# Optimization experiments

Hardware: AMD Instinct MI355X
Metric: run time of the kernel (lower is better)

Reference implementation:

```python
import jax, jax.numpy as jnp
import numpy as np

MARGIN = 0.2
SIMILARITY_WEIGHT = 1.0
PD_EPS = 1e-6   # F.pairwise_distance eps (added to the difference)
COS_EPS = 1e-8  # F.cosine_similarity eps (norm clamp)

B, D = 8192, 256


def setup_inputs() -> dict:
    key = jax.random.key(0)
    k1, k2, k3, k4 = jax.random.split(key, 4)
    anchor = jax.random.normal(k1, (B, D), dtype=jnp.float32)
    positive = jax.random.normal(k2, (B, D), dtype=jnp.float32)
    negative = jax.random.normal(k3, (B, D), dtype=jnp.float32)
    similarity_matrix = jax.random.uniform(k4, (B, B), dtype=jnp.float32)
    return {"anchor": anchor, "positive": positive, "negative": negative,
            "similarity_matrix": similarity_matrix}


def reference(anchor, positive, negative, similarity_matrix):
    # Triplet term: F.pairwise_distance(x1, x2, p=2, eps=1e-6) = ||x1 - x2 + eps||_2
    d_pos = jnp.linalg.norm(anchor - positive + PD_EPS, axis=1)  # [B]
    d_neg = jnp.linalg.norm(anchor - negative + PD_EPS, axis=1)  # [B]
    triplet = jnp.mean(jax.nn.relu(d_pos - d_neg + MARGIN))

    # Pairwise cosine similarity of anchor rows (vectorized matmul form).
    norms = jnp.linalg.norm(anchor, axis=1, keepdims=True)       # [B,1]
    a_hat = anchor / jnp.maximum(norms, COS_EPS)                 # [B,D]
    cos = a_hat @ a_hat.T                                        # [B,B]

    # sum_{i,j} mse(cos_ij, S_ij) / B^2 == mean((cos - S)^2)
    sim_loss = jnp.mean((cos - similarity_matrix) ** 2)

    return triplet + SIMILARITY_WEIGHT * sim_loss
```

## Files before the change

kernel.cpp:

```cpp
#include <hip/hip_runtime.h>
#include <hip/hip_bf16.h>

#define BDIM 8192
#define DDIM 256

typedef __attribute__((ext_vector_type(8))) short  s16x8;
typedef __attribute__((ext_vector_type(4))) float  f32x4;

#define GLOBAL_AS __attribute__((address_space(1)))
#define LDS_AS    __attribute__((address_space(3)))

__device__ __forceinline__ void stage16(const float* g, float* l) {
    __builtin_amdgcn_global_load_lds((const GLOBAL_AS unsigned int*)g,
                                     (LDS_AS unsigned int*)l, 16, 0, 0);
}

__device__ inline ushort f2bf(float x) {
    __hip_bfloat16 h = __float2bfloat16(x);
    ushort u;
    __builtin_memcpy(&u, &h, 2);
    return u;
}

__global__ __launch_bounds__(256) void row_stats(
    const float* __restrict__ A, const float* __restrict__ P,
    const float* __restrict__ N, ushort* __restrict__ Asw,
    float* __restrict__ partial_trip)
{
    __shared__ float tsh[4];
    const int wave = threadIdx.x >> 6;
    const int lane = threadIdx.x & 63;
    const int row  = blockIdx.x * 4 + wave;

    const float4 a = *(reinterpret_cast<const float4*>(A + (size_t)row * DDIM) + lane);
    const float4 p = *(reinterpret_cast<const float4*>(P + (size_t)row * DDIM) + lane);
    const float4 n = *(reinterpret_cast<const float4*>(N + (size_t)row * DDIM) + lane);

    float sa = a.x*a.x + a.y*a.y + a.z*a.z + a.w*a.w;

    float d0 = a.x - p.x + 1e-6f, d1 = a.y - p.y + 1e-6f;
    float d2 = a.z - p.z + 1e-6f, d3 = a.w - p.w + 1e-6f;
    float sp = d0*d0 + d1*d1 + d2*d2 + d3*d3;

    d0 = a.x - n.x + 1e-6f; d1 = a.y - n.y + 1e-6f;
    d2 = a.z - n.z + 1e-6f; d3 = a.w - n.w + 1e-6f;
    float sn = d0*d0 + d1*d1 + d2*d2 + d3*d3;

    #pragma unroll
    for (int off = 32; off > 0; off >>= 1) {
        sa += __shfl_xor(sa, off);
        sp += __shfl_xor(sp, off);
        sn += __shfl_xor(sn, off);
    }

    const float inv = 1.0f / fmaxf(sqrtf(sa), 1e-8f);

    ushort4 hv;
    hv.x = f2bf(a.x * inv);
    hv.y = f2bf(a.y * inv);
    hv.z = f2bf(a.z * inv);
    hv.w = f2bf(a.w * inv);
    const size_t chunk = ((size_t)(row >> 4) * 8 + (lane >> 3)) * 64
                       + (size_t)(((lane >> 1) & 3) * 16 + (row & 15));
    *reinterpret_cast<ushort4*>(Asw + chunk * 8 + (lane & 1) * 4) = hv;

    if (lane == 0)
        tsh[wave] = fmaxf(sqrtf(sp) - sqrtf(sn) + 0.2f, 0.0f);
    __syncthreads();
    if (threadIdx.x == 0)
        partial_trip[blockIdx.x] = tsh[0] + tsh[1] + tsh[2] + tsh[3];
}

__global__ __launch_bounds__(256) void cos_mse(
    const ushort* __restrict__ Asw,
    const float* __restrict__ S, float* __restrict__ partial_sim)
{
    __shared__ float s_tile[128 * 128];
    __shared__ float wsum[4];

    const int tid  = threadIdx.x;
    const int w    = tid >> 6;
    const int lane = tid & 63;

    const int bid = blockIdx.x;
    const int swz = (bid & 7) * 512 + (bid >> 3);
    const int ti  = (swz >> 6) * 128;
    const int tj  = (swz & 63) * 128;

    {
        const int rhalf = lane >> 5;
        const int col16 = lane & 31;
        const float* gsrc = S + (size_t)(ti + w * 2 + rhalf) * BDIM + tj + col16 * 4;
        #pragma unroll
        for (int it = 0; it < 16; ++it)
            stage16(gsrc + (size_t)it * 8 * BDIM, &s_tile[(it * 8 + w * 2) * 128]);
    }

    const int wr = (w >> 1) * 64;
    const int wc = (w & 1) * 64;
    const int fr = lane & 15;
    const int kg = lane >> 4;

    const ushort* ab = Asw + (size_t)((ti + wr) >> 4) * 4096 + (size_t)lane * 8;
    const ushort* bb = Asw + (size_t)((tj + wc) >> 4) * 4096 + (size_t)lane * 8;

    f32x4 acc[4][4] = {};

    #pragma unroll 2
    for (int k32 = 0; k32 < 8; ++k32) {
        s16x8 af[4], bf4[4];
        #pragma unroll
        for (int m = 0; m < 4; ++m)
            af[m] = *reinterpret_cast<const s16x8*>(ab + m * 4096 + k32 * 512);
        #pragma unroll
        for (int n = 0; n < 4; ++n)
            bf4[n] = *reinterpret_cast<const s16x8*>(bb + n * 4096 + k32 * 512);
        #pragma unroll
        for (int m = 0; m < 4; ++m)
            #pragma unroll
            for (int n = 0; n < 4; ++n)
                acc[m][n] = __builtin_amdgcn_mfma_f32_16x16x32_bf16(
                    af[m], bf4[n], acc[m][n], 0, 0, 0);
    }

    __syncthreads();

    float local = 0.0f;
    #pragma unroll
    for (int m = 0; m < 4; ++m) {
        #pragma unroll
        for (int reg = 0; reg < 4; ++reg) {
            const int lr = wr + m * 16 + kg * 4 + reg;
            #pragma unroll
            for (int n = 0; n < 4; ++n) {
                const float d = acc[m][n][reg] - s_tile[lr * 128 + wc + n * 16 + fr];
                local += d * d;
            }
        }
    }

    #pragma unroll
    for (int off = 32; off > 0; off >>= 1)
        local += __shfl_down(local, off);
    if (lane == 0) wsum[w] = local;
    __syncthreads();
    if (tid == 0)
        partial_sim[bid] = wsum[0] + wsum[1] + wsum[2] + wsum[3];
}

__global__ __launch_bounds__(256) void finalize(
    const float* __restrict__ pt, const float* __restrict__ ps,
    float* __restrict__ out)
{
    __shared__ float sh[4];
    float v = 0.0f;
    for (int i = threadIdx.x; i < 2048; i += 256) v += pt[i] * (1.0f / (float)BDIM);
    for (int i = threadIdx.x; i < 4096; i += 256)
        v += ps[i] * (1.0f / ((float)BDIM * (float)BDIM));
    #pragma unroll
    for (int off = 32; off > 0; off >>= 1) v += __shfl_down(v, off);
    const int w = threadIdx.x >> 6, lane = threadIdx.x & 63;
    if (lane == 0) sh[w] = v;
    __syncthreads();
    if (threadIdx.x == 0) out[0] = sh[0] + sh[1] + sh[2] + sh[3];
}

extern "C" void kernel_launch(void* const* d_in, const int* in_sizes, int n_in,
                              void* d_out, int out_size, void* d_ws, size_t ws_size,
                              hipStream_t stream)
{
    const float* anchor   = (const float*)d_in[0];
    const float* positive = (const float*)d_in[1];
    const float* negative = (const float*)d_in[2];
    const float* S        = (const float*)d_in[3];
    float* out = (float*)d_out;

    float*  partial_trip = (float*)d_ws;
    float*  partial_sim  = (float*)d_ws + 2048;
    ushort* Asw          = (ushort*)((char*)d_ws + 32768);

    row_stats<<<BDIM / 4, 256, 0, stream>>>(anchor, positive, negative, Asw, partial_trip);
    cos_mse<<<4096, 256, 0, stream>>>(Asw, S, partial_sim);
    finalize<<<1, 256, 0, stream>>>(partial_trip, partial_sim, out);
}
```

Before: 111.9 us.

## Make cos_mse persistent over 8 column tiles, keeping A fragments in registers

The cos_mse kernel now launches 512 blocks, and each block loops over 8 column tiles of the same 128-row band. The row band's A fragments (32 bf16x8 registers) are loaded once and reused across all 8 tiles. S tile staging now uses a nontemporal cache hint, launch bounds request 2 blocks per SIMD, and partial sums are written per wave so finalize reduces 16384 values. The S load for each tile is not overlapped with the previous tile's compute, and the extra register pressure may lower occupancy. There are also fewer blocks to hide latency.

```diff
diff --git a/kernel.cpp b/kernel.cpp
--- a/kernel.cpp
+++ b/kernel.cpp
@@ -10,9 +10,9 @@
 #define GLOBAL_AS __attribute__((address_space(1)))
 #define LDS_AS    __attribute__((address_space(3)))
 
-__device__ __forceinline__ void stage16(const float* g, float* l) {
+__device__ __forceinline__ void stage16nt(const float* g, float* l) {
     __builtin_amdgcn_global_load_lds((const GLOBAL_AS unsigned int*)g,
-                                     (LDS_AS unsigned int*)l, 16, 0, 0);
+                                     (LDS_AS unsigned int*)l, 16, 0, 2 );
 }
 
 __device__ inline ushort f2bf(float x) {
@@ -71,81 +71,92 @@
         partial_trip[blockIdx.x] = tsh[0] + tsh[1] + tsh[2] + tsh[3];
 }
 
-__global__ __launch_bounds__(256) void cos_mse(
+__global__ __launch_bounds__(256, 2) void cos_mse(
     const ushort* __restrict__ Asw,
-    const float* __restrict__ S, float* __restrict__ partial_sim)
+    const float* __restrict__ S,
+    float* __restrict__ partial_sim)
 {
     __shared__ float s_tile[128 * 128];
-    __shared__ float wsum[4];
 
     const int tid  = threadIdx.x;
     const int w    = tid >> 6;
     const int lane = tid & 63;
 
-    const int bid = blockIdx.x;
-    const int swz = (bid & 7) * 512 + (bid >> 3);
-    const int ti  = (swz >> 6) * 128;
-    const int tj  = (swz & 63) * 128;
+    const int b   = blockIdx.x;
+    const int xcd = b & 7;
+    const int q   = b >> 3;
+    const int ti  = (xcd * 8 + (q >> 3)) * 128;
 
+    const int wr    = (w >> 1) * 64;
+    const int wc    = (w & 1) * 64;
+    const int fr    = lane & 15;
+    const int kg    = lane >> 4;
+    const int rhalf = lane >> 5;
+    const int col16 = lane & 31;
+
+    s16x8 af[32];
     {
-        const int rhalf = lane >> 5;
-        const int col16 = lane & 31;
-        const float* gsrc = S + (size_t)(ti + w * 2 + rhalf) * BDIM + tj + col16 * 4;
+        const ushort* ab = Asw + (size_t)((ti + wr) >> 4) * 4096 + (size_t)lane * 8;
         #pragma unroll
-        for (int it = 0; it < 16; ++it)
-            stage16(gsrc + (size_t)it * 8 * BDIM, &s_tile[(it * 8 + w * 2) * 128]);
+        for (int k32 = 0; k32 < 8; ++k32)
+            #pragma unroll
+            for (int m = 0; m < 4; ++m)
+                af[k32 * 4 + m] = *reinterpret_cast<const s16x8*>(
+                    ab + (size_t)m * 4096 + k32 * 512);
     }
 
-    const int wr = (w >> 1) * 64;
-    const int wc = (w & 1) * 64;
-    const int fr = lane & 15;
-    const int kg = lane >> 4;
+    for (int i = 0; i < 8; ++i) {
+        const int tj = ((q & 7) * 8 + i) * 128;
 
-    const ushort* ab = Asw + (size_t)((ti + wr) >> 4) * 4096 + (size_t)lane * 8;
-    const ushort* bb = Asw + (size_t)((tj + wc) >> 4) * 4096 + (size_t)lane * 8;
+        {
+            const float* gsrc = S + (size_t)(ti + w * 2 + rhalf) * BDIM + tj + col16 * 4;
+            #pragma unroll
+            for (int it = 0; it < 16; ++it)
+                stage16nt(gsrc + (size_t)it * 8 * BDIM,
+                          &s_tile[(it * 8 + w * 2) * 128]);
+        }
 
-    f32x4 acc[4][4] = {};
+        f32x4 acc[4][4] = {};
+        const ushort* bb = Asw + (size_t)((tj + wc) >> 4) * 4096 + (size_t)lane * 8;
+        #pragma unroll
+        for (int k32 = 0; k32 < 8; ++k32) {
+            s16x8 bf4[4];
+            #pragma unroll
+            for (int n = 0; n < 4; ++n)
+                bf4[n] = *reinterpret_cast<const s16x8*>(
+                    bb + (size_t)n * 4096 + k32 * 512);
+            #pragma unroll
+            for (int m = 0; m < 4; ++m)
+                #pragma unroll
+                for (int n = 0; n < 4; ++n)
+                    acc[m][n] = __builtin_amdgcn_mfma_f32_16x16x32_bf16(
+                        af[k32 * 4 + m], bf4[n], acc[m][n], 0, 0, 0);
+        }
 
-    #pragma unroll 2
-    for (int k32 = 0; k32 < 8; ++k32) {
-        s16x8 af[4], bf4[4];
-        #pragma unroll
-        for (int m = 0; m < 4; ++m)
-            af[m] = *reinterpret_cast<const s16x8*>(ab + m * 4096 + k32 * 512);
-        #pragma unroll
-        for (int n = 0; n < 4; ++n)
-            bf4[n] = *reinterpret_cast<const s16x8*>(bb + n * 4096 + k32 * 512);
+        __syncthreads();
+
+        float local = 0.0f;
         #pragma unroll
         for (int m = 0; m < 4; ++m)
             #pragma unroll
-            for (int n = 0; n < 4; ++n)
-                acc[m][n] = __builtin_amdgcn_mfma_f32_16x16x32_bf16(
-                    af[m], bf4[n], acc[m][n], 0, 0, 0);
+            for (int reg = 0; reg < 4; ++reg) {
+                const int lr = wr + m * 16 + kg * 4 + reg;
+                #pragma unroll
+                for (int n = 0; n < 4; ++n) {
+                    const float d = acc[m][n][reg]
+                                  - s_tile[lr * 128 + wc + n * 16 + fr];
+                    local += d * d;
+                }
+            }
+
+        #pragma unroll
+        for (int off = 32; off > 0; off >>= 1)
+            local += __shfl_down(local, off);
+        if (lane == 0)
+            partial_sim[(size_t)(xcd * 512 + q * 8 + i) * 4 + w] = local;
+
+        __syncthreads();
     }
-
-    __syncthreads();
-
-    float local = 0.0f;
-    #pragma unroll
-    for (int m = 0; m < 4; ++m) {
-        #pragma unroll
-        for (int reg = 0; reg < 4; ++reg) {
-            const int lr = wr + m * 16 + kg * 4 + reg;
-            #pragma unroll
-            for (int n = 0; n < 4; ++n) {
-                const float d = acc[m][n][reg] - s_tile[lr * 128 + wc + n * 16 + fr];
-                local += d * d;
-            }
-        }
-    }
-
-    #pragma unroll
-    for (int off = 32; off > 0; off >>= 1)
-        local += __shfl_down(local, off);
-    if (lane == 0) wsum[w] = local;
-    __syncthreads();
-    if (tid == 0)
-        partial_sim[bid] = wsum[0] + wsum[1] + wsum[2] + wsum[3];
 }
 
 __global__ __launch_bounds__(256) void finalize(
@@ -154,8 +165,9 @@
 {
     __shared__ float sh[4];
     float v = 0.0f;
-    for (int i = threadIdx.x; i < 2048; i += 256) v += pt[i] * (1.0f / (float)BDIM);
-    for (int i = threadIdx.x; i < 4096; i += 256)
+    for (int i = threadIdx.x; i < 2048; i += 256)
+        v += pt[i] * (1.0f / (float)BDIM);
+    for (int i = threadIdx.x; i < 16384; i += 256)
         v += ps[i] * (1.0f / ((float)BDIM * (float)BDIM));
     #pragma unroll
     for (int off = 32; off > 0; off >>= 1) v += __shfl_down(v, off);
@@ -176,10 +188,10 @@
     float* out = (float*)d_out;
 
     float*  partial_trip = (float*)d_ws;
-    float*  partial_sim  = (float*)d_ws + 2048;
-    ushort* Asw          = (ushort*)((char*)d_ws + 32768);
+    float*  partial_sim  = (float*)((char*)d_ws + 8192);
+    ushort* Asw          = (ushort*)((char*)d_ws + 131072);
 
     row_stats<<<BDIM / 4, 256, 0, stream>>>(anchor, positive, negative, Asw, partial_trip);
-    cos_mse<<<4096, 256, 0, stream>>>(Asw, S, partial_sim);
+    cos_mse<<<512, 256, 0, stream>>>(Asw, S, partial_sim);
     finalize<<<1, 256, 0, stream>>>(partial_trip, partial_sim, out);
 }
```

Result: faster. 100.4 us (-10.3%).

## Expand MSE algebraically into Gram Frobenius norm, S·A dot, and S²

Applied to the files above, without the earlier changes.

Replaces the direct cos-minus-S tile computation with the identity sum((AAᵀ−S)²) = ||AᵀA||_F² − 2·tr(Aᵀ S A) + ||S||². A transpose kernel builds a K-major bf16 copy of the normalized anchors. A split-K gram kernel plus a reduction computes the 256×256 AᵀA. A streaming s_dot kernel multiplies bf16-converted S tiles by Â, dots the result with Â and accumulates S² in the same pass. This removes the B×B×D cosine GEMM in favor of a B×B×D S·Â GEMM that streams S once. The cost is more launches, bf16 rounding of S, and cancellation between large terms that may hurt accuracy.

```diff
diff --git a/kernel.cpp b/kernel.cpp
--- a/kernel.cpp
+++ b/kernel.cpp
@@ -6,14 +6,6 @@
 
 typedef __attribute__((ext_vector_type(8))) short  s16x8;
 typedef __attribute__((ext_vector_type(4))) float  f32x4;
-
-#define GLOBAL_AS __attribute__((address_space(1)))
-#define LDS_AS    __attribute__((address_space(3)))
-
-__device__ __forceinline__ void stage16(const float* g, float* l) {
-    __builtin_amdgcn_global_load_lds((const GLOBAL_AS unsigned int*)g,
-                                     (LDS_AS unsigned int*)l, 16, 0, 0);
-}
 
 __device__ inline ushort f2bf(float x) {
     __hip_bfloat16 h = __float2bfloat16(x);
@@ -71,98 +63,236 @@
         partial_trip[blockIdx.x] = tsh[0] + tsh[1] + tsh[2] + tsh[3];
 }
 
-__global__ __launch_bounds__(256) void cos_mse(
-    const ushort* __restrict__ Asw,
-    const float* __restrict__ S, float* __restrict__ partial_sim)
-{
-    __shared__ float s_tile[128 * 128];
-    __shared__ float wsum[4];
-
-    const int tid  = threadIdx.x;
-    const int w    = tid >> 6;
-    const int lane = tid & 63;
-
-    const int bid = blockIdx.x;
-    const int swz = (bid & 7) * 512 + (bid >> 3);
-    const int ti  = (swz >> 6) * 128;
-    const int tj  = (swz & 63) * 128;
-
-    {
-        const int rhalf = lane >> 5;
-        const int col16 = lane & 31;
-        const float* gsrc = S + (size_t)(ti + w * 2 + rhalf) * BDIM + tj + col16 * 4;
-        #pragma unroll
-        for (int it = 0; it < 16; ++it)
-            stage16(gsrc + (size_t)it * 8 * BDIM, &s_tile[(it * 8 + w * 2) * 128]);
-    }
-
-    const int wr = (w >> 1) * 64;
-    const int wc = (w & 1) * 64;
-    const int fr = lane & 15;
-    const int kg = lane >> 4;
-
-    const ushort* ab = Asw + (size_t)((ti + wr) >> 4) * 4096 + (size_t)lane * 8;
-    const ushort* bb = Asw + (size_t)((tj + wc) >> 4) * 4096 + (size_t)lane * 8;
-
-    f32x4 acc[4][4] = {};
-
-    #pragma unroll 2
+__global__ __launch_bounds__(256) void transpose_ahat(
+    const ushort* __restrict__ Asw, ushort* __restrict__ Asw2)
+{
+    const int t = threadIdx.x, w = t >> 6, lane = t & 63;
+    const int fr = lane & 15, kg = lane >> 4;
+    const int b = blockIdx.x;
+    const int j0 = b * 128 + w * 32;
+
+    #pragma unroll 1
+    for (int D = 0; D < 16; ++D) {
+        const int d = D * 16 + fr;
+        ushort v[8];
+        #pragma unroll
+        for (int jj = 0; jj < 8; ++jj) {
+            const int J = j0 + kg * 8 + jj;
+            v[jj] = Asw[(size_t)(J >> 4) * 4096 + (d >> 5) * 512
+                        + ((d >> 3) & 3) * 128 + (J & 15) * 8 + (d & 7)];
+        }
+        uint4 pk;
+        pk.x = v[0] | ((unsigned)v[1] << 16);
+        pk.y = v[2] | ((unsigned)v[3] << 16);
+        pk.z = v[4] | ((unsigned)v[5] << 16);
+        pk.w = v[6] | ((unsigned)v[7] << 16);
+        *reinterpret_cast<uint4*>(
+            Asw2 + (size_t)(D * 256 + b * 4 + w) * 512 + (size_t)lane * 8) = pk;
+    }
+}
+
+__global__ __launch_bounds__(256, 2) void gram(
+    const ushort* __restrict__ Asw2, float* __restrict__ Mpart)
+{
+    const int t = threadIdx.x, w = t >> 6, lane = t & 63;
+    const int fr = lane & 15, kg = lane >> 4;
+    const int kc = blockIdx.x;
+    const int h  = blockIdx.y;
+
+    f32x4 acc[8][4] = {};
+    #pragma unroll 1
     for (int k32 = 0; k32 < 8; ++k32) {
-        s16x8 af[4], bf4[4];
-        #pragma unroll
-        for (int m = 0; m < 4; ++m)
-            af[m] = *reinterpret_cast<const s16x8*>(ab + m * 4096 + k32 * 512);
+        const int j5 = (kc * 256 + k32 * 32) >> 5;
+        s16x8 af[8], bf[4];
+        #pragma unroll
+        for (int m = 0; m < 8; ++m)
+            af[m] = *reinterpret_cast<const s16x8*>(
+                Asw2 + ((size_t)((h * 8 + m) * 256 + j5)) * 512 + lane * 8);
         #pragma unroll
         for (int n = 0; n < 4; ++n)
-            bf4[n] = *reinterpret_cast<const s16x8*>(bb + n * 4096 + k32 * 512);
-        #pragma unroll
-        for (int m = 0; m < 4; ++m)
+            bf[n] = *reinterpret_cast<const s16x8*>(
+                Asw2 + ((size_t)((w * 4 + n) * 256 + j5)) * 512 + lane * 8);
+        #pragma unroll
+        for (int m = 0; m < 8; ++m)
             #pragma unroll
             for (int n = 0; n < 4; ++n)
                 acc[m][n] = __builtin_amdgcn_mfma_f32_16x16x32_bf16(
-                    af[m], bf4[n], acc[m][n], 0, 0, 0);
-    }
-
+                    af[m], bf[n], acc[m][n], 0, 0, 0);
+    }
+    float* base = Mpart + (size_t)kc * 65536
+                + (size_t)(h * 128 + kg * 4) * 256 + w * 64 + fr;
+    #pragma unroll
+    for (int m = 0; m < 8; ++m)
+        #pragma unroll
+        for (int reg = 0; reg < 4; ++reg)
+            #pragma unroll
+            for (int n = 0; n < 4; ++n)
+                base[(size_t)(m * 16 + reg) * 256 + n * 16] = acc[m][n][reg];
+}
+
+__global__ __launch_bounds__(256) void gram_reduce(
+    const float* __restrict__ Mpart, float* __restrict__ gpart)
+{
+    __shared__ float sh[4];
+    const int t = threadIdx.x;
+    const int id = blockIdx.x * 256 + t;
+    float ss = 0.f;
+    for (int e = id; e < 65536; e += 16384) {
+        float s = 0.f;
+        #pragma unroll 4
+        for (int kc = 0; kc < 32; ++kc)
+            s += Mpart[(size_t)kc * 65536 + e];
+        ss += s * s;
+    }
+    #pragma unroll
+    for (int off = 32; off > 0; off >>= 1) ss += __shfl_down(ss, off);
+    const int w = t >> 6, lane = t & 63;
+    if (lane == 0) sh[w] = ss;
     __syncthreads();
-
-    float local = 0.0f;
-    #pragma unroll
-    for (int m = 0; m < 4; ++m) {
-        #pragma unroll
-        for (int reg = 0; reg < 4; ++reg) {
-            const int lr = wr + m * 16 + kg * 4 + reg;
+    if (t == 0) gpart[blockIdx.x] = sh[0] + sh[1] + sh[2] + sh[3];
+}
+
+__global__ __launch_bounds__(512, 2) void s_dot(
+    const float* __restrict__ S, const ushort* __restrict__ Asw,
+    const ushort* __restrict__ Asw2,
+    float* __restrict__ dotp, float* __restrict__ s2p)
+{
+    __shared__ ushort sbuf[2][128 * 64];
+    __shared__ float red[16];
+
+    const int t = threadIdx.x;
+    const int w = t >> 6, lane = t & 63;
+    const int fr = lane & 15, kg = lane >> 4;
+
+    const int bid = blockIdx.x;
+    const int ti  = (bid >> 2) * 128;
+    const int c0  = (bid & 3) * 2048;
+
+    const int srow = t >> 2, sq = t & 3;
+    const float* sg = S + (size_t)(ti + srow) * BDIM + c0 + sq * 4;
+
+    float s2_local = 0.f;
+    f32x4 acc[8][2] = {};
+    float4 sv[4];
+    s16x8 bcur[4], bnxt[4];
+
+    auto load_round = [&](int r) {
+        #pragma unroll
+        for (int i = 0; i < 4; ++i)
+            sv[i] = *reinterpret_cast<const float4*>(sg + (size_t)r * 64 + i * 16);
+    };
+    auto bfrag = [&](int n, int j) {
+        return *reinterpret_cast<const s16x8*>(
+            Asw2 + ((size_t)((w * 2 + n) * 256 + (j >> 5))) * 512 + lane * 8);
+    };
+    auto stage_write = [&](int buf) {
+        ushort* dst = &sbuf[buf][srow * 64];
+        #pragma unroll
+        for (int i = 0; i < 4; ++i) {
+            s2_local += sv[i].x*sv[i].x + sv[i].y*sv[i].y
+                      + sv[i].z*sv[i].z + sv[i].w*sv[i].w;
+            uint2 pk;
+            pk.x = f2bf(sv[i].x) | ((unsigned)f2bf(sv[i].y) << 16);
+            pk.y = f2bf(sv[i].z) | ((unsigned)f2bf(sv[i].w) << 16);
+            const int c = i * 2 + (sq >> 1);
+            *reinterpret_cast<uint2*>(
+                dst + ((c ^ (srow & 7)) * 8) + (sq & 1) * 4) = pk;
+        }
+    };
+
+    load_round(0);
+    stage_write(0);
+    bcur[0] = bfrag(0, c0);      bcur[1] = bfrag(1, c0);
+    bcur[2] = bfrag(0, c0 + 32); bcur[3] = bfrag(1, c0 + 32);
+    __builtin_amdgcn_sched_barrier(0);
+    load_round(1);
+    __builtin_amdgcn_sched_barrier(0);
+    asm volatile("s_waitcnt lgkmcnt(0)" ::: "memory");
+    __builtin_amdgcn_sched_barrier(0);
+    __builtin_amdgcn_s_barrier();
+
+    for (int r = 0; r < 32; ++r) {
+        const int buf = r & 1;
+        #pragma unroll
+        for (int kk = 0; kk < 2; ++kk)
             #pragma unroll
-            for (int n = 0; n < 4; ++n) {
-                const float d = acc[m][n][reg] - s_tile[lr * 128 + wc + n * 16 + fr];
-                local += d * d;
+            for (int m = 0; m < 8; ++m) {
+                const int R = m * 16 + fr;
+                const s16x8 a = *reinterpret_cast<const s16x8*>(
+                    &sbuf[buf][R * 64 + (((kk * 4 + kg) ^ (R & 7)) * 8)]);
+                acc[m][0] = __builtin_amdgcn_mfma_f32_16x16x32_bf16(
+                    a, bcur[kk * 2 + 0], acc[m][0], 0, 0, 0);
+                acc[m][1] = __builtin_amdgcn_mfma_f32_16x16x32_bf16(
+                    a, bcur[kk * 2 + 1], acc[m][1], 0, 0, 0);
+            }
+        if (r < 31) {
+            const int jn = c0 + (r + 1) * 64;
+            bnxt[0] = bfrag(0, jn);      bnxt[1] = bfrag(1, jn);
+            bnxt[2] = bfrag(0, jn + 32); bnxt[3] = bfrag(1, jn + 32);
+            __builtin_amdgcn_sched_barrier(0);
+            stage_write(buf ^ 1);
+            if (r < 30)
+                load_round(r + 2);
+            __builtin_amdgcn_sched_barrier(0);
+            asm volatile("s_waitcnt lgkmcnt(0)" ::: "memory");
+            __builtin_amdgcn_sched_barrier(0);
+            __builtin_amdgcn_s_barrier();
+            bcur[0] = bnxt[0]; bcur[1] = bnxt[1];
+            bcur[2] = bnxt[2]; bcur[3] = bnxt[3];
+        }
+    }
+
+    float dot_local = 0.f;
+    #pragma unroll 1
+    for (int m = 0; m < 8; ++m) {
+        #pragma unroll
+        for (int n = 0; n < 2; ++n) {
+            const int d = w * 32 + n * 16 + fr;
+            const size_t abase = (size_t)((ti >> 4) + m) * 4096
+                               + (d >> 5) * 512 + ((d >> 3) & 3) * 128 + (d & 7);
+            #pragma unroll
+            for (int reg = 0; reg < 4; ++reg) {
+                const ushort u = Asw[abase + (kg * 4 + reg) * 8];
+                dot_local += __uint_as_float((unsigned)u << 16) * acc[m][n][reg];
             }
         }
     }
 
     #pragma unroll
-    for (int off = 32; off > 0; off >>= 1)
-        local += __shfl_down(local, off);
-    if (lane == 0) wsum[w] = local;
+    for (int off = 32; off > 0; off >>= 1) {
+        dot_local += __shfl_down(dot_local, off);
+        s2_local  += __shfl_down(s2_local, off);
+    }
+    if (lane == 0) { red[w] = dot_local; red[8 + w] = s2_local; }
     __syncthreads();
-    if (tid == 0)
-        partial_sim[bid] = wsum[0] + wsum[1] + wsum[2] + wsum[3];
+    if (t == 0) {
+        float da = 0.f, sb = 0.f;
+        #pragma unroll
+        for (int i = 0; i < 8; ++i) { da += red[i]; sb += red[8 + i]; }
+        dotp[bid] = da;
+        s2p[bid]  = sb;
+    }
 }
 
 __global__ __launch_bounds__(256) void finalize(
-    const float* __restrict__ pt, const float* __restrict__ ps,
+    const float* __restrict__ pt, const float* __restrict__ dotp,
+    const float* __restrict__ s2p, const float* __restrict__ gpart,
     float* __restrict__ out)
 {
     __shared__ float sh[4];
-    float v = 0.0f;
-    for (int i = threadIdx.x; i < 2048; i += 256) v += pt[i] * (1.0f / (float)BDIM);
-    for (int i = threadIdx.x; i < 4096; i += 256)
-        v += ps[i] * (1.0f / ((float)BDIM * (float)BDIM));
+    const int t = threadIdx.x;
+    float trip = 0.f, sim = 0.f;
+    for (int i = t; i < 2048; i += 256) trip += pt[i];
+    sim += -2.f * dotp[t] + s2p[t];
+    if (t < 64) sim += gpart[t];
+    float v = trip * (1.0f / (float)BDIM)
+            + sim  * (1.0f / ((float)BDIM * (float)BDIM));
     #pragma unroll
     for (int off = 32; off > 0; off >>= 1) v += __shfl_down(v, off);
-    const int w = threadIdx.x >> 6, lane = threadIdx.x & 63;
+    const int w = t >> 6, lane = t & 63;
     if (lane == 0) sh[w] = v;
     __syncthreads();
-    if (threadIdx.x == 0) out[0] = sh[0] + sh[1] + sh[2] + sh[3];
+    if (t == 0) out[0] = sh[0] + sh[1] + sh[2] + sh[3];
 }
 
 extern "C" void kernel_launch(void* const* d_in, const int* in_sizes, int n_in,
@@ -175,11 +305,18 @@
     const float* S        = (const float*)d_in[3];
     float* out = (float*)d_out;
 
-    float*  partial_trip = (float*)d_ws;
-    float*  partial_sim  = (float*)d_ws + 2048;
-    ushort* Asw          = (ushort*)((char*)d_ws + 32768);
-
-    row_stats<<<BDIM / 4, 256, 0, stream>>>(anchor, positive, negative, Asw, partial_trip);
-    cos_mse<<<4096, 256, 0, stream>>>(Asw, S, partial_sim);
-    finalize<<<1, 256, 0, stream>>>(partial_trip, partial_sim, out);
-}
+    float*  pt    = (float*)d_ws;
+    float*  dotp  = (float*)((char*)d_ws + 8192);
+    float*  s2p   = (float*)((char*)d_ws + 12288);
+    float*  gpart = (float*)((char*)d_ws + 16384);
+    ushort* Asw   = (ushort*)((char*)d_ws + (1u  << 20));
+    ushort* Asw2  = (ushort*)((char*)d_ws + (8u  << 20));
+    float*  Mpart = (float*)((char*)d_ws + (16u << 20));
+
+    row_stats<<<BDIM / 4, 256, 0, stream>>>(anchor, positive, negative, Asw, pt);
+    transpose_ahat<<<64, 256, 0, stream>>>(Asw, Asw2);
+    gram<<<dim3(32, 2), 256, 0, stream>>>(Asw2, Mpart);
+    gram_reduce<<<64, 256, 0, stream>>>(Mpart, gpart);
+    s_dot<<<256, 512, 0, stream>>>(S, Asw, Asw2, dotp, s2p);
+    finalize<<<1, 256, 0, stream>>>(pt, dotp, s2p, gpart, out);
+}
```

Result: slower. 146.5 us (+30.9%).
